# Kernel tuning notes

Measured on AMD Instinct MI355X. Metric: run time of the kernel, lower is better.

Reference implementation:

```python
import jax, jax.numpy as jnp
import numpy as np
from jax import lax

B, S, E, H, V, L = 16, 256, 256, 256, 50000, 9


def setup_inputs() -> dict:
    key = jax.random.key(0)
    ks = jax.random.split(key, 12)
    s = 0.05
    return {
        "input_ids": jax.random.randint(ks[0], (B, S), 0, V),
        "attention_mask": jnp.ones((B, S), dtype=jnp.int32),
        "labels": jax.random.randint(ks[1], (B, S), 0, L),
        "embedding": jax.random.normal(ks[2], (V, E), jnp.float32) * s,
        "w_ih_l0": jax.random.normal(ks[3], (2, 4 * H, E), jnp.float32) * s,
        "w_ih_rest": jax.random.normal(ks[4], (3, 2, 4 * H, 2 * H), jnp.float32) * s,
        "w_hh": jax.random.normal(ks[5], (4, 2, 4 * H, H), jnp.float32) * s,
        "b": jax.random.normal(ks[6], (4, 2, 2, 4 * H), jnp.float32) * s,
        "ln_g": jnp.ones((2 * H,), jnp.float32),
        "ln_b": jnp.zeros((2 * H,), jnp.float32),
        "lin_w": jax.random.normal(ks[7], (L, 2 * H), jnp.float32) * s,
        "lin_b": jnp.zeros((L,), jnp.float32),
        "crf_start": jax.random.normal(ks[8], (L,), jnp.float32) * s,
        "crf_end": jax.random.normal(ks[9], (L,), jnp.float32) * s,
        "crf_trans": jax.random.normal(ks[10], (L, L), jnp.float32) * s,
    }


def _lstm_dir(x, w_ih, w_hh, b_ih, b_hh, reverse):
    # x: [B,S,in]; PyTorch gate order i,f,g,o packed along 4H.
    Bb = x.shape[0]
    Hh = w_hh.shape[1]
    xg = jnp.einsum('bsi,gi->bsg', x, w_ih) + b_ih + b_hh  # precompute input projection
    if reverse:
        xg = xg[:, ::-1]

    def step(carry, g):
        h, c = carry
        g = g + h @ w_hh.T
        i, f, gg, o = jnp.split(g, 4, axis=-1)
        c = jax.nn.sigmoid(f) * c + jax.nn.sigmoid(i) * jnp.tanh(gg)
        h = jax.nn.sigmoid(o) * jnp.tanh(c)
        return (h, c), h

    z = jnp.zeros((Bb, Hh), x.dtype)
    _, hs = lax.scan(step, (z, z), jnp.swapaxes(xg, 0, 1))
    hs = jnp.swapaxes(hs, 0, 1)  # [B,S,H]
    if reverse:
        hs = hs[:, ::-1]
    return hs


def _forward(input_ids, attention_mask, labels, embedding, w_ih_l0, w_ih_rest,
             w_hh, b, ln_g, ln_b, lin_w, lin_b, crf_start, crf_end, crf_trans):
    x = embedding[input_ids]  # [B,S,E]
    for layer in range(4):
        wf = w_ih_l0[0] if layer == 0 else w_ih_rest[layer - 1, 0]
        wb = w_ih_l0[1] if layer == 0 else w_ih_rest[layer - 1, 1]
        hf = _lstm_dir(x, wf, w_hh[layer, 0], b[layer, 0, 0], b[layer, 0, 1], False)
        hb = _lstm_dir(x, wb, w_hh[layer, 1], b[layer, 1, 0], b[layer, 1, 1], True)
        x = jnp.concatenate([hf, hb], axis=-1)  # [B,S,2H]
    # dropout is identity in eval mode
    mu = x.mean(-1, keepdims=True)
    var = ((x - mu) ** 2).mean(-1, keepdims=True)
    x = (x - mu) * lax.rsqrt(var + 1e-5) * ln_g + ln_b
    logits = jnp.einsum('bsh,lh->bsl', x, lin_w) + lin_b  # emissions [B,S,L]

    # CRF negative log-likelihood (torchcrf semantics, reduction='sum')
    Bb = logits.shape[0]
    mask_f = attention_mask.astype(logits.dtype)
    bidx = jnp.arange(Bb)
    first = labels[:, 0]
    num = crf_start[first] + logits[bidx, 0, first]
    em_t = jnp.swapaxes(logits, 0, 1)[1:]  # [S-1,B,L]
    tprev = labels[:, :-1].T
    tcur = labels[:, 1:].T
    mt = mask_f[:, 1:].T

    def num_step(s, inp):
        e, tp, tc, m = inp
        return s + (crf_trans[tp, tc] + e[bidx, tc]) * m, None

    num, _ = lax.scan(num_step, num, (em_t, tprev, tcur, mt))
    last = jnp.sum(attention_mask, axis=1).astype(jnp.int32) - 1
    num = num + crf_end[labels[bidx, last]]

    alpha = crf_start + logits[:, 0]  # [B,L]

    def den_step(a, inp):
        e, m = inp
        nxt = jax.nn.logsumexp(a[:, :, None] + crf_trans[None] + e[:, None, :], axis=1)
        return jnp.where(m[:, None] > 0, nxt, a), None

    alpha, _ = lax.scan(den_step, alpha, (em_t, mt))
    denom = jax.nn.logsumexp(alpha + crf_end, axis=-1)
    loss = -(num - denom).sum()
    return logits, loss


def reference(input_ids, attention_mask, labels, embedding, w_ih_l0, w_ih_rest,
              w_hh, b, ln_g, ln_b, lin_w, lin_b, crf_start, crf_end, crf_trans):
    return _forward(input_ids, attention_mask, labels, embedding, w_ih_l0,
                    w_ih_rest, w_hh, b, ln_g, ln_b, lin_w, lin_b,
                    crf_start, crf_end, crf_trans)
```

## Files before the change

kernel.cpp:

```cpp
#include <hip/hip_runtime.h>
#include <math.h>

#define BB 16
#define SS 256
#define LL 9
#define ROWS 4096
#define APITCH 40
#define HP 272

typedef __attribute__((ext_vector_type(8))) short short8;
typedef __attribute__((ext_vector_type(4))) float f32x4;
typedef __attribute__((ext_vector_type(8))) int i32x8;

#define HSCALE 256.0f
#define LOG2E  1.44269504f
#define WCONST 1477.3199f
#define SCALE_ONE 0x7F7F7F7Fu
#define SCALE_IFO 0x6D6D6D6Du
#define SCALE_G   0x6E6E6E6Eu

__device__ __forceinline__ unsigned short f2bf(float f) {
  unsigned u = __float_as_uint(f);
  return (unsigned short)((u + 0x7FFF + ((u >> 16) & 1)) >> 16);
}
__device__ __forceinline__ float bf2f(unsigned short s) {
  return __uint_as_float(((unsigned)s) << 16);
}

__global__ __launch_bounds__(256) void embed_bf16(
    const int* __restrict__ ids, const float* __restrict__ emb,
    unsigned short* __restrict__ x0) {
  int row = blockIdx.x;
  int id = ids[row];
  x0[(size_t)row * 256 + threadIdx.x] = f2bf(emb[(size_t)id * 256 + threadIdx.x]);
}

__global__ __launch_bounds__(64) void pack_whh_mx(
    const float* __restrict__ w, unsigned* __restrict__ wfrag) {
  int nb = blockIdx.x, ks2 = blockIdx.y, z = blockIdx.z;
  int lane = threadIdx.x, qq = lane >> 4, col = lane & 15;
  int g = nb >> 4;
  float csc = (g == 2) ? WCONST : -WCONST;
  const float* wp = w + (size_t)z * 1024 * 256 + (size_t)(nb * 16 + col) * 256 +
                    ks2 * 128 + qq * 32;
  unsigned* op = wfrag + (((size_t)(z * 64 + nb) * 2 + ks2) * 64 + lane) * 8;
#pragma unroll
  for (int u = 0; u < 8; ++u) {
    float v0 = wp[u * 4 + 0] * csc, v1 = wp[u * 4 + 1] * csc;
    float v2 = wp[u * 4 + 2] * csc, v3 = wp[u * 4 + 3] * csc;
    unsigned pk = __builtin_amdgcn_cvt_pk_fp8_f32(v0, v1, 0, false);
    pk = __builtin_amdgcn_cvt_pk_fp8_f32(v2, v3, pk, true);
    op[u] = pk;
  }
}

__global__ __launch_bounds__(256) void bias_perm(
    const float* __restrict__ b2, float* __restrict__ biasP) {
  int i = blockIdx.x * 256 + threadIdx.x;
  int l = i >> 11, r = i & 2047;
  int dir = r >> 10, np = r & 1023;
  int n = ((np & 3) << 8) + (np >> 2);
  biasP[i] = b2[l * 4096 + dir * 2048 + n] + b2[l * 4096 + dir * 2048 + 1024 + n];
}

__global__ __launch_bounds__(256) void gemm_xg_bf16(
    const unsigned short* __restrict__ A, int K,
    const float* __restrict__ Wih,
    const float* __restrict__ biasP,
    unsigned short* __restrict__ xgP) {
  int dir = blockIdx.z;
  const float* Bw = Wih + (size_t)dir * 1024 * K;
  int n0 = blockIdx.x * 64, m0 = blockIdx.y * 64;
  int tid = threadIdx.x;
  int wv = tid >> 6, lane = tid & 63, quad = lane >> 4, col = lane & 15;
  __shared__ unsigned short As[64 * APITCH];
  __shared__ unsigned short Bs[64 * APITCH];
  int lr = tid >> 2;
  int lk = (tid & 3) * 8;
  int nprime = n0 + lr;
  int nphys = ((nprime & 3) << 8) + (nprime >> 2);
  f32x4 acc[4];
#pragma unroll
  for (int nt = 0; nt < 4; ++nt) acc[nt] = (f32x4){0.f, 0.f, 0.f, 0.f};

  for (int k0 = 0; k0 < K; k0 += 32) {
    short8 av = *(const short8*)&A[(size_t)(m0 + lr) * K + k0 + lk];
    float4 b0 = *(const float4*)&Bw[(size_t)nphys * K + k0 + lk];
    float4 b1 = *(const float4*)&Bw[(size_t)nphys * K + k0 + lk + 4];
    short8 bv;
    bv[0] = (short)f2bf(b0.x); bv[1] = (short)f2bf(b0.y);
    bv[2] = (short)f2bf(b0.z); bv[3] = (short)f2bf(b0.w);
    bv[4] = (short)f2bf(b1.x); bv[5] = (short)f2bf(b1.y);
    bv[6] = (short)f2bf(b1.z); bv[7] = (short)f2bf(b1.w);
    __syncthreads();
    *(short8*)&As[lr * APITCH + lk] = av;
    *(short8*)&Bs[lr * APITCH + lk] = bv;
    __syncthreads();
    short8 af = *(const short8*)&As[(wv * 16 + col) * APITCH + quad * 8];
#pragma unroll
    for (int nt = 0; nt < 4; ++nt) {
      short8 bf = *(const short8*)&Bs[(nt * 16 + col) * APITCH + quad * 8];
      acc[nt] = __builtin_amdgcn_mfma_f32_16x16x32_bf16(af, bf, acc[nt], 0, 0, 0);
    }
  }
#pragma unroll
  for (int nt = 0; nt < 4; ++nt) {
    int np = n0 + nt * 16 + col;
    float bia = biasP[dir * 1024 + np];
    float cg = ((np & 3) == 2) ? (2.0f * LOG2E) : (-LOG2E);
#pragma unroll
    for (int r = 0; r < 4; ++r) {
      int row = m0 + wv * 16 + quad * 4 + r;
      xgP[((size_t)dir * ROWS + row) * 1024 + np] = f2bf((acc[nt][r] + bia) * cg);
    }
  }
}

__global__ __launch_bounds__(512, 2) void lstm_mx(
    const unsigned short* __restrict__ xgP,
    const unsigned* __restrict__ wfrag,
    unsigned short* __restrict__ xout) {
  int dir = blockIdx.x & 1;
  int bg = blockIdx.x >> 1;
  int tid = threadIdx.x;
  int wv = tid >> 6, lane = tid & 63;
  int quad = lane >> 4, col = lane & 15;

  __shared__ __align__(16) unsigned char Hfrag[2][2 * HP];

  {
    int* hz = (int*)&Hfrag[0][0];
    for (int i = tid; i < HP; i += 512) hz[i] = 0;
  }

  i32x8 wf[2][4][2];
#pragma unroll
  for (int hbi = 0; hbi < 2; ++hbi)
#pragma unroll
    for (int g = 0; g < 4; ++g) {
      int nb = g * 16 + 2 * wv + hbi;
#pragma unroll
      for (int ks2 = 0; ks2 < 2; ++ks2)
        wf[hbi][g][ks2] = *(const i32x8*)(wfrag +
            (((size_t)(dir * 64 + nb) * 2 + ks2) * 64 + lane) * 8);
    }

  int aoff = ((lane & 15) >> 3) * HP + (lane >> 4) * 32;

  int hbsel = quad & 1;
  int bq = quad >> 1;
  int j = 32 * wv + 16 * hbsel + col;
  int b = bg * 2 + bq;
  int pos0 = dir ? (SS - 1) : 0;
  int dstep = dir ? -1 : 1;
  const unsigned short* xq_ptr =
      xgP + ((size_t)dir * ROWS + (size_t)b * SS + pos0) * 1024 + j * 4;
  unsigned short* xo_ptr = xout + ((size_t)b * SS + pos0) * 512 + dir * 256 + j;
  int xq_d = dstep * 1024;
  int xo_d = dstep * 512;
  int hw = bq * HP + j;

  float Cp = 0.f;
  unsigned short ph = 0;
  unsigned short* xo_prev = xo_ptr;
  int cur = 0;
  __syncthreads();

  for (int t = 0; t < SS; ++t) {
    if (t) *xo_prev = ph;
    ushort4 xq = *(const ushort4*)xq_ptr;
    xq_ptr += xq_d;

    i32x8 af0 = *(const i32x8*)&Hfrag[cur][aoff];
    i32x8 af1 = *(const i32x8*)&Hfrag[cur][aoff + 128];
    f32x4 acc[2][4];
#pragma unroll
    for (int hbi = 0; hbi < 2; ++hbi) {
#pragma unroll
      for (int g = 0; g < 4; ++g) {
        f32x4 a = (f32x4){0.f, 0.f, 0.f, 0.f};
        a = __builtin_amdgcn_mfma_scale_f32_16x16x128_f8f6f4(
                af0, wf[hbi][g][0], a, 0, 0, 0, SCALE_ONE, 0,
                (g == 2) ? SCALE_G : SCALE_IFO);
        a = __builtin_amdgcn_mfma_scale_f32_16x16x128_f8f6f4(
                af1, wf[hbi][g][1], a, 0, 0, 0, SCALE_ONE, 0,
                (g == 2) ? SCALE_G : SCALE_IFO);
        acc[hbi][g] = a;
      }
    }

    int nxt = cur ^ 1;
    float a_i = hbsel ? acc[1][0][0] : acc[0][0][0];
    float a_f = hbsel ? acc[1][1][0] : acc[0][1][0];
    float a_g = hbsel ? acc[1][2][0] : acc[0][2][0];
    float a_o = hbsel ? acc[1][3][0] : acc[0][3][0];
    float gi = a_i + bf2f(xq.x);
    float gf = a_f + bf2f(xq.y);
    float gt = a_g + bf2f(xq.z);
    float go = a_o + bf2f(xq.w);
    float si = __builtin_amdgcn_rcpf(1.0f + __builtin_amdgcn_exp2f(gi));
    float sf = __builtin_amdgcn_rcpf(1.0f + __builtin_amdgcn_exp2f(gf));
    float so = __builtin_amdgcn_rcpf(1.0f + __builtin_amdgcn_exp2f(go));
    float rg = __builtin_amdgcn_rcpf(1.0f + __builtin_amdgcn_exp2f(gt));
    float tg2 = fmaf(-4.0f * LOG2E, rg, 2.0f * LOG2E);
    Cp = fmaf(sf, Cp, si * tg2);
    float rc = __builtin_amdgcn_rcpf(1.0f + __builtin_amdgcn_exp2f(Cp));
    float h = so * fmaf(-2.0f, rc, 1.0f);
    unsigned pk = __builtin_amdgcn_cvt_pk_fp8_f32(h * HSCALE, h * HSCALE, 0, false);
    Hfrag[nxt][hw] = (unsigned char)(pk & 0xFF);
    ph = f2bf(h);
    xo_prev = xo_ptr;
    xo_ptr += xo_d;
    __syncthreads();
    cur = nxt;
  }
  *xo_prev = ph;
}

__global__ __launch_bounds__(64) void ln_logits(
    const unsigned short* __restrict__ X, const float* __restrict__ g,
    const float* __restrict__ bt, const float* __restrict__ W,
    const float* __restrict__ lb, float* __restrict__ out) {
  int row = blockIdx.x;
  int lane = threadIdx.x;
  const unsigned short* x = X + (size_t)row * 512;
  float v[8];
  float s = 0.f, s2 = 0.f;
#pragma unroll
  for (int i = 0; i < 8; ++i) {
    v[i] = bf2f(x[lane + 64 * i]);
    s += v[i];
    s2 += v[i] * v[i];
  }
#pragma unroll
  for (int off = 32; off; off >>= 1) {
    s += __shfl_down(s, off, 64);
    s2 += __shfl_down(s2, off, 64);
  }
  s = __shfl(s, 0, 64);
  s2 = __shfl(s2, 0, 64);
  float mu = s * (1.f / 512.f);
  float var = s2 * (1.f / 512.f) - mu * mu;
  float rstd = rsqrtf(var + 1e-5f);
  float y[8];
#pragma unroll
  for (int i = 0; i < 8; ++i) {
    int e = lane + 64 * i;
    y[i] = (v[i] - mu) * rstd * g[e] + bt[e];
  }
  for (int l = 0; l < LL; ++l) {
    float p = 0.f;
#pragma unroll
    for (int i = 0; i < 8; ++i) p += y[i] * W[(size_t)l * 512 + lane + 64 * i];
#pragma unroll
    for (int off = 32; off; off >>= 1) p += __shfl_down(p, off, 64);
    if (lane == 0) out[(size_t)row * LL + l] = p + lb[l];
  }
}

__global__ __launch_bounds__(256) void crf_kernel(
    const float* __restrict__ logits, const int* __restrict__ labels,
    const int* __restrict__ mask, const float* __restrict__ cs,
    const float* __restrict__ ce, const float* __restrict__ ct,
    float* __restrict__ loss_out) {
  __shared__ float trans[9][12];
  __shared__ float alpha[2][BB][12];
  __shared__ float numsh[BB];
  __shared__ float res[BB];
  int tid = threadIdx.x;
  int b = tid >> 4;
  int i = tid & 15;
  if (tid < 81) trans[tid / 9][tid % 9] = ct[tid];
  __syncthreads();
  const float* lg = logits + (size_t)b * SS * LL;
  const int* lbp = labels + (size_t)b * SS;
  const int* mk = mask + (size_t)b * SS;

  float np = 0.f;
  int msum = 0;
  for (int t = i; t < SS; t += 16) {
    msum += mk[t];
    if (t == 0) {
      int l0 = lbp[0];
      np += cs[l0] + lg[l0];
    } else {
      float m = (float)mk[t];
      np += (trans[lbp[t - 1]][lbp[t]] + lg[(size_t)t * LL + lbp[t]]) * m;
    }
  }
#pragma unroll
  for (int off = 8; off; off >>= 1) {
    np += __shfl_down(np, off, 16);
    msum += __shfl_down(msum, off, 16);
  }
  if (i == 0) {
    int last = msum - 1;
    numsh[b] = np + ce[lbp[last]];
  }

  if (i < LL) alpha[0][b][i] = cs[i] + lg[i];
  int cur = 0;
  for (int t = 1; t < SS; ++t) {
    if (i < LL) {
      float e = lg[(size_t)t * LL + i];
      float av[9];
      float mmax = -1e30f;
#pragma unroll
      for (int p = 0; p < LL; ++p) {
        float vv = alpha[cur][b][p] + trans[p][i];
        av[p] = vv;
        mmax = fmaxf(mmax, vv);
      }
      float ssum = 0.f;
#pragma unroll
      for (int p = 0; p < LL; ++p) ssum += __expf(av[p] - mmax);
      float anew = e + mmax + logf(ssum);
      float aold = alpha[cur][b][i];
      alpha[cur ^ 1][b][i] = (mk[t] > 0) ? anew : aold;
    }
    cur ^= 1;
  }
  if (i == 0) {
    float arr[9];
    float m2 = -1e30f;
#pragma unroll
    for (int cc = 0; cc < LL; ++cc) {
      arr[cc] = alpha[cur][b][cc] + ce[cc];
      m2 = fmaxf(m2, arr[cc]);
    }
    float ssd = 0.f;
#pragma unroll
    for (int cc = 0; cc < LL; ++cc) ssd += __expf(arr[cc] - m2);
    float denom = m2 + logf(ssd);
    res[b] = numsh[b] - denom;
  }
  __syncthreads();
  if (tid == 0) {
    float Lsum = 0.f;
    for (int b2 = 0; b2 < BB; ++b2) Lsum += res[b2];
    loss_out[0] = -Lsum;
  }
}

extern "C" void kernel_launch(void* const* d_in, const int* in_sizes, int n_in,
                              void* d_out, int out_size, void* d_ws, size_t ws_size,
                              hipStream_t stream) {
  const int* input_ids = (const int*)d_in[0];
  const int* attn_mask = (const int*)d_in[1];
  const int* labels = (const int*)d_in[2];
  const float* embedding = (const float*)d_in[3];
  const float* w_ih_l0 = (const float*)d_in[4];
  const float* w_ih_rest = (const float*)d_in[5];
  const float* w_hh = (const float*)d_in[6];
  const float* bvec = (const float*)d_in[7];
  const float* ln_g = (const float*)d_in[8];
  const float* ln_b = (const float*)d_in[9];
  const float* lin_w = (const float*)d_in[10];
  const float* lin_b = (const float*)d_in[11];
  const float* crf_start = (const float*)d_in[12];
  const float* crf_end = (const float*)d_in[13];
  const float* crf_trans = (const float*)d_in[14];
  float* out = (float*)d_out;
  char* base = (char*)d_ws;

  unsigned short* x0    = (unsigned short*)(base);
  unsigned short* xoutA = (unsigned short*)(base + (2u << 20));
  unsigned short* xoutB = (unsigned short*)(base + (6u << 20));
  unsigned short* xgP   = (unsigned short*)(base + (10u << 20));
  unsigned*       wfrag = (unsigned*)(base + (26u << 20));
  float*          biasP = (float*)(base + (28u << 20));

  embed_bf16<<<ROWS, 256, 0, stream>>>(input_ids, embedding, x0);
  pack_whh_mx<<<dim3(64, 2, 8), 64, 0, stream>>>(w_hh, wfrag);
  bias_perm<<<32, 256, 0, stream>>>(bvec, biasP);

  const unsigned short* cur = x0;
  unsigned short* nxt = xoutA;
  for (int l = 0; l < 4; ++l) {
    int K = l ? 512 : 256;
    const float* wih = l ? (w_ih_rest + (size_t)(l - 1) * 2 * 1024 * 512) : w_ih_l0;
    gemm_xg_bf16<<<dim3(16, 64, 2), 256, 0, stream>>>(
        cur, K, wih, biasP + (size_t)l * 2048, xgP);
    lstm_mx<<<16, 512, 0, stream>>>(xgP, wfrag + (size_t)l * 131072, nxt);
    cur = nxt;
    nxt = (nxt == xoutA) ? xoutB : xoutA;
  }

  ln_logits<<<ROWS, 64, 0, stream>>>(cur, ln_g, ln_b, lin_w, lin_b, out);
  crf_kernel<<<1, 256, 0, stream>>>(out, labels, attn_mask, crf_start, crf_end,
                                    crf_trans, out + (size_t)ROWS * LL);
}
```

Baseline: 1.216 ms.

## Pre-pack input weights to bf16 and use 128x128 GEMM with direct LDS loads

Adds a prep kernel that converts and permutes W_ih to bf16 once, folding the gate scale into both weights and bias. The input-projection GEMM moves to 128x128 tiles with 8 waves, each wave computing a 64x32 sub-tile, and fills LDS through global_load_lds. This removes per-tile fp32-to-bf16 conversion and raises data reuse per tile. The cost is an extra prep launch and memory pass, fewer blocks (512 instead of 2048), and an unpadded LDS layout that may cause bank conflicts.

```diff
diff --git a/kernel.cpp b/kernel.cpp
--- a/kernel.cpp
+++ b/kernel.cpp
@@ -1,11 +1,11 @@
 #include <hip/hip_runtime.h>
 #include <math.h>
+#include <stdint.h>
 
 #define BB 16
 #define SS 256
 #define LL 9
 #define ROWS 4096
-#define APITCH 40
 #define HP 272
 
 typedef __attribute__((ext_vector_type(8))) short short8;
@@ -25,6 +25,12 @@
 }
 __device__ __forceinline__ float bf2f(unsigned short s) {
   return __uint_as_float(((unsigned)s) << 16);
+}
+
+__device__ __forceinline__ void gl2lds16(const void* g, void* l) {
+  __builtin_amdgcn_global_load_lds(
+      (const __attribute__((address_space(1))) void*)g,
+      (__attribute__((address_space(3))) void*)l, 16, 0, 0);
 }
 
 __global__ __launch_bounds__(256) void embed_bf16(
@@ -55,63 +61,89 @@
 }
 
 __global__ __launch_bounds__(256) void bias_perm(
-    const float* __restrict__ b2, float* __restrict__ biasP) {
+    const float* __restrict__ b2, float* __restrict__ biasPF) {
   int i = blockIdx.x * 256 + threadIdx.x;
   int l = i >> 11, r = i & 2047;
   int dir = r >> 10, np = r & 1023;
   int n = ((np & 3) << 8) + (np >> 2);
-  biasP[i] = b2[l * 4096 + dir * 2048 + n] + b2[l * 4096 + dir * 2048 + 1024 + n];
-}
-
-__global__ __launch_bounds__(256) void gemm_xg_bf16(
+  float cg = ((np & 3) == 2) ? (2.0f * LOG2E) : (-LOG2E);
+  biasPF[i] = (b2[l * 4096 + dir * 2048 + n] + b2[l * 4096 + dir * 2048 + 1024 + n]) * cg;
+}
+
+__global__ __launch_bounds__(256) void prep_wih(
+    const float* __restrict__ w_l0, const float* __restrict__ w_rest,
+    unsigned short* __restrict__ wp, const long* __restrict__ woff_dummy) {
+  int l = blockIdx.z;
+  int Ksh = l ? 9 : 8;
+  int K = 1 << Ksh;
+  long total = (long)2 * 1024 * K;
+  long idx = (long)blockIdx.x * 256 + threadIdx.x;
+  if (idx >= total) return;
+  int k = (int)(idx & (K - 1));
+  long r = idx >> Ksh;
+  int np = (int)(r & 1023), dir = (int)(r >> 10);
+  int nph = ((np & 3) << 8) + (np >> 2);
+  float cg = ((np & 3) == 2) ? (2.0f * LOG2E) : (-LOG2E);
+  const float* src = l ? (w_rest + (size_t)(l - 1) * 2 * 1024 * 512) : w_l0;
+  size_t off = l ? (524288 + (size_t)(l - 1) * 1048576) : 0;
+  wp[off + idx] = f2bf(src[((size_t)dir * 1024 + nph) * K + k] * cg);
+}
+
+__global__ __launch_bounds__(512) void gemm_xg128(
     const unsigned short* __restrict__ A, int K,
-    const float* __restrict__ Wih,
-    const float* __restrict__ biasP,
+    const unsigned short* __restrict__ BP,
+    const float* __restrict__ biasPF,
     unsigned short* __restrict__ xgP) {
   int dir = blockIdx.z;
-  const float* Bw = Wih + (size_t)dir * 1024 * K;
-  int n0 = blockIdx.x * 64, m0 = blockIdx.y * 64;
+  int n0 = blockIdx.x * 128, m0 = blockIdx.y * 128;
   int tid = threadIdx.x;
   int wv = tid >> 6, lane = tid & 63, quad = lane >> 4, col = lane & 15;
-  __shared__ unsigned short As[64 * APITCH];
-  __shared__ unsigned short Bs[64 * APITCH];
-  int lr = tid >> 2;
-  int lk = (tid & 3) * 8;
-  int nprime = n0 + lr;
-  int nphys = ((nprime & 3) << 8) + (nprime >> 2);
-  f32x4 acc[4];
-#pragma unroll
-  for (int nt = 0; nt < 4; ++nt) acc[nt] = (f32x4){0.f, 0.f, 0.f, 0.f};
+  __shared__ unsigned short As[128 * 32];
+  __shared__ unsigned short Bs[128 * 32];
+  const unsigned short* Bw = BP + (size_t)dir * 1024 * K;
+
+  int srow = lane >> 2;
+  int scol = (lane & 3) * 8;
+  const unsigned short* ga = A + (size_t)(m0 + wv * 16 + srow) * K + scol;
+  const unsigned short* gb = Bw + (size_t)(n0 + wv * 16 + srow) * K + scol;
+  unsigned short* lA = &As[wv * 512];
+  unsigned short* lB = &Bs[wv * 512];
+
+  int wm = wv & 1;
+  int wn = wv >> 1;
+  f32x4 acc[4][2];
+#pragma unroll
+  for (int mt = 0; mt < 4; ++mt)
+#pragma unroll
+    for (int nt = 0; nt < 2; ++nt) acc[mt][nt] = (f32x4){0.f, 0.f, 0.f, 0.f};
 
   for (int k0 = 0; k0 < K; k0 += 32) {
-    short8 av = *(const short8*)&A[(size_t)(m0 + lr) * K + k0 + lk];
-    float4 b0 = *(const float4*)&Bw[(size_t)nphys * K + k0 + lk];
-    float4 b1 = *(const float4*)&Bw[(size_t)nphys * K + k0 + lk + 4];
-    short8 bv;
-    bv[0] = (short)f2bf(b0.x); bv[1] = (short)f2bf(b0.y);
-    bv[2] = (short)f2bf(b0.z); bv[3] = (short)f2bf(b0.w);
-    bv[4] = (short)f2bf(b1.x); bv[5] = (short)f2bf(b1.y);
-    bv[6] = (short)f2bf(b1.z); bv[7] = (short)f2bf(b1.w);
     __syncthreads();
-    *(short8*)&As[lr * APITCH + lk] = av;
-    *(short8*)&Bs[lr * APITCH + lk] = bv;
+    gl2lds16(ga, lA);
+    gl2lds16(gb, lB);
+    ga += 32; gb += 32;
     __syncthreads();
-    short8 af = *(const short8*)&As[(wv * 16 + col) * APITCH + quad * 8];
-#pragma unroll
-    for (int nt = 0; nt < 4; ++nt) {
-      short8 bf = *(const short8*)&Bs[(nt * 16 + col) * APITCH + quad * 8];
-      acc[nt] = __builtin_amdgcn_mfma_f32_16x16x32_bf16(af, bf, acc[nt], 0, 0, 0);
-    }
-  }
-#pragma unroll
-  for (int nt = 0; nt < 4; ++nt) {
-    int np = n0 + nt * 16 + col;
-    float bia = biasP[dir * 1024 + np];
-    float cg = ((np & 3) == 2) ? (2.0f * LOG2E) : (-LOG2E);
-#pragma unroll
-    for (int r = 0; r < 4; ++r) {
-      int row = m0 + wv * 16 + quad * 4 + r;
-      xgP[((size_t)dir * ROWS + row) * 1024 + np] = f2bf((acc[nt][r] + bia) * cg);
+    short8 bf0 = *(const short8*)&Bs[(wn * 32 + col) * 32 + quad * 8];
+    short8 bf1 = *(const short8*)&Bs[(wn * 32 + 16 + col) * 32 + quad * 8];
+#pragma unroll
+    for (int mt = 0; mt < 4; ++mt) {
+      short8 af = *(const short8*)&As[(wm * 64 + mt * 16 + col) * 32 + quad * 8];
+      acc[mt][0] = __builtin_amdgcn_mfma_f32_16x16x32_bf16(af, bf0, acc[mt][0], 0, 0, 0);
+      acc[mt][1] = __builtin_amdgcn_mfma_f32_16x16x32_bf16(af, bf1, acc[mt][1], 0, 0, 0);
+    }
+  }
+
+#pragma unroll
+  for (int nt = 0; nt < 2; ++nt) {
+    int np = n0 + wn * 32 + nt * 16 + col;
+    float bia = biasPF[dir * 1024 + np];
+#pragma unroll
+    for (int mt = 0; mt < 4; ++mt) {
+#pragma unroll
+      for (int r = 0; r < 4; ++r) {
+        int row = m0 + wm * 64 + mt * 16 + quad * 4 + r;
+        xgP[((size_t)dir * ROWS + row) * 1024 + np] = f2bf(acc[mt][nt][r] + bia);
+      }
     }
   }
 }
@@ -368,19 +400,22 @@
   unsigned short* xoutB = (unsigned short*)(base + (6u << 20));
   unsigned short* xgP   = (unsigned short*)(base + (10u << 20));
   unsigned*       wfrag = (unsigned*)(base + (26u << 20));
-  float*          biasP = (float*)(base + (28u << 20));
+  float*          biasPF= (float*)(base + (28u << 20));
+  unsigned short* wihP  = (unsigned short*)(base + (29u << 20));
 
   embed_bf16<<<ROWS, 256, 0, stream>>>(input_ids, embedding, x0);
   pack_whh_mx<<<dim3(64, 2, 8), 64, 0, stream>>>(w_hh, wfrag);
-  bias_perm<<<32, 256, 0, stream>>>(bvec, biasP);
+  bias_perm<<<32, 256, 0, stream>>>(bvec, biasPF);
+  prep_wih<<<dim3(4096, 1, 4), 256, 0, stream>>>(w_ih_l0, w_ih_rest, wihP, nullptr);
+
+  const size_t WOFF[4] = {0, 524288, 1572864, 2621440};
 
   const unsigned short* cur = x0;
   unsigned short* nxt = xoutA;
   for (int l = 0; l < 4; ++l) {
     int K = l ? 512 : 256;
-    const float* wih = l ? (w_ih_rest + (size_t)(l - 1) * 2 * 1024 * 512) : w_ih_l0;
-    gemm_xg_bf16<<<dim3(16, 64, 2), 256, 0, stream>>>(
-        cur, K, wih, biasP + (size_t)l * 2048, xgP);
+    gemm_xg128<<<dim3(8, 32, 2), 512, 0, stream>>>(
+        cur, K, wihP + WOFF[l], biasPF + (size_t)l * 2048, xgP);
     lstm_mx<<<16, 512, 0, stream>>>(xgP, wfrag + (size_t)l * 131072, nxt);
     cur = nxt;
     nxt = (nxt == xoutA) ? xoutB : xoutA;
```

After: 1.198 ms. No clear change (-1.4%).
